# Kernel optimization log

Hardware: AMD Instinct MI355X
Metric: run time of the kernel (lower is better)

Reference implementation:

```python
import jax, jax.numpy as jnp
import numpy as np

N_NODES = 50000
N_EDGES = 800000
IN_FEATS = 128
H_FEATS = 256


def setup_inputs() -> dict:
    key = jax.random.key(0)
    ks = jax.random.split(key, 10)
    in_feat = jax.random.normal(ks[0], (N_NODES, IN_FEATS), dtype=jnp.float32)
    src = jax.random.randint(ks[1], (N_EDGES,), 0, N_NODES, dtype=jnp.int32)
    dst = jax.random.randint(ks[2], (N_EDGES,), 0, N_NODES, dtype=jnp.int32)
    s1 = 1.0 / np.sqrt(IN_FEATS)
    s2 = 1.0 / np.sqrt(H_FEATS)
    return {
        "in_feat": in_feat,
        "src": src,
        "dst": dst,
        "W_self1": jax.random.normal(ks[3], (IN_FEATS, H_FEATS), dtype=jnp.float32) * s1,
        "W_neigh1": jax.random.normal(ks[4], (IN_FEATS, H_FEATS), dtype=jnp.float32) * s1,
        "b1": jnp.zeros((H_FEATS,), dtype=jnp.float32),
        "W_self2": jax.random.normal(ks[5], (H_FEATS, H_FEATS), dtype=jnp.float32) * s2,
        "W_neigh2": jax.random.normal(ks[6], (H_FEATS, H_FEATS), dtype=jnp.float32) * s2,
        "b2": jnp.zeros((H_FEATS,), dtype=jnp.float32),
    }


def _sage_conv(h, src, dst, W_self, W_neigh, b, deg_inv):
    # gather neighbor features along edges, mean-reduce into dst nodes
    msg = h[src]                                              # [E, d]
    agg = jax.ops.segment_sum(msg, dst, num_segments=N_NODES)  # [N, d]
    h_neigh = agg * deg_inv                                   # mean aggregation
    return h @ W_self + h_neigh @ W_neigh + b


def reference(in_feat, src, dst, W_self1, W_neigh1, b1, W_self2, W_neigh2, b2):
    # in-degree for mean (zero-degree nodes -> 0 neighbor contribution)
    deg = jax.ops.segment_sum(jnp.ones((N_EDGES,), dtype=jnp.float32), dst,
                              num_segments=N_NODES)
    deg_inv = (1.0 / jnp.maximum(deg, 1.0))[:, None]          # [N, 1]
    h = _sage_conv(in_feat, src, dst, W_self1, W_neigh1, b1, deg_inv)
    h = jax.nn.relu(h)
    h = _sage_conv(h, src, dst, W_self2, W_neigh2, b2, deg_inv)
    return h
```

## Files before the change

### kernel.cpp

```cpp
#include <hip/hip_runtime.h>
#include <hip/hip_bf16.h>
#include <stdint.h>

#define NN 50000
#define NE 800000
#define IN_F 128
#define H_F 256
#define M_PAD 50048

typedef unsigned int uint32;
typedef unsigned short u16;
typedef __attribute__((ext_vector_type(8))) short short8;
typedef __attribute__((ext_vector_type(4))) float floatx4;

__device__ __forceinline__ float bf16_to_f(uint32 bits16) {
    union { uint32 u; float f; } c; c.u = bits16 << 16; return c.f;
}
__device__ __forceinline__ uint32 f_to_bf16(float f) {
    union { float f; uint32 u; } c; c.f = f;
    uint32 u = c.u;
    u += 0x7FFFu + ((u >> 16) & 1u);
    return u >> 16;
}

__device__ __forceinline__ void gload_lds16(const void* g, void* l) {
    __builtin_amdgcn_global_load_lds((__attribute__((address_space(1))) void*)g,
                                     (__attribute__((address_space(3))) void*)l,
                                     16, 0, 0);
}

#define PREP_A (NN * IN_F / 4)
#define PREP_B (256 * 256)
#define PREP_C (256 * 512)
#define PREP_Z (16 + 32)
#define PREP_TOTAL (PREP_A + PREP_B + PREP_C + PREP_Z + NE)

__global__ void prep_kernel(const float* __restrict__ in_feat, u16* __restrict__ inA,
                            const float* __restrict__ Ws1, const float* __restrict__ Wn1,
                            u16* __restrict__ BT1,
                            const float* __restrict__ Ws2, const float* __restrict__ Wn2,
                            u16* __restrict__ BT2,
                            u16* __restrict__ h,
                            const int* __restrict__ dst, int* __restrict__ counts,
                            int* __restrict__ rank) {
    int id = blockIdx.x * 256 + threadIdx.x;
    if (id < PREP_A) {
        float4 v = *((const float4*)in_feat + id);
        ushort4 o;
        o.x = (u16)f_to_bf16(v.x); o.y = (u16)f_to_bf16(v.y);
        o.z = (u16)f_to_bf16(v.z); o.w = (u16)f_to_bf16(v.w);
        *((ushort4*)inA + id) = o;
        return;
    }
    id -= PREP_A;
    if (id < PREP_B) {
        int n = id >> 8, k = id & 255;
        float v = (k < 128) ? Ws1[(size_t)k * H_F + n] : Wn1[(size_t)(k - 128) * H_F + n];
        BT1[(size_t)n * 256 + k] = (u16)f_to_bf16(v);
        return;
    }
    id -= PREP_B;
    if (id < PREP_C) {
        int n = id >> 9, k = id & 511;
        float v = (k < 256) ? Ws2[(size_t)k * H_F + n] : Wn2[(size_t)(k - 256) * H_F + n];
        BT2[(size_t)n * 512 + k] = (u16)f_to_bf16(v);
        return;
    }
    id -= PREP_C;
    if (id < PREP_Z) {
        uint4 z = {0u, 0u, 0u, 0u};
        if (id < 16) *((uint4*)(inA + (size_t)NN * IN_F) + id) = z;
        else         *((uint4*)(h   + (size_t)NN * H_F)  + (id - 16)) = z;
        return;
    }
    id -= PREP_Z;
    if (id < NE) rank[id] = atomicAdd(&counts[dst[id]], 1);
}


__global__ void scan1_kernel(const int* __restrict__ counts, int* __restrict__ row_start,
                             int* __restrict__ partials, int n) {
    __shared__ int s[256];
    int t = threadIdx.x;
    int i = blockIdx.x * 256 + t;
    int x = (i < n) ? counts[i] : 0;
    s[t] = x;
    __syncthreads();
    for (int off = 1; off < 256; off <<= 1) {
        int y = (t >= off) ? s[t - off] : 0;
        __syncthreads();
        s[t] += y;
        __syncthreads();
    }
    if (i < n) row_start[i] = s[t] - x;
    if (t == 255) partials[blockIdx.x] = s[255];
}

__global__ void scan2_kernel(int* __restrict__ partials, int n) {
    __shared__ int s[256];
    int t = threadIdx.x;
    int x = (t < n) ? partials[t] : 0;
    s[t] = x;
    __syncthreads();
    for (int off = 1; off < 256; off <<= 1) {
        int y = (t >= off) ? s[t - off] : 0;
        __syncthreads();
        s[t] += y;
        __syncthreads();
    }
    if (t < n) partials[t] = s[t] - x;
}

__global__ void scan3_kernel(int* __restrict__ row_start, const int* __restrict__ partials,
                             const int* __restrict__ counts,
                             float* __restrict__ deg_inv, int n) {
    int i = blockIdx.x * 256 + threadIdx.x;
    if (i >= n) return;
    row_start[i] += partials[blockIdx.x];
    int c = counts[i];
    deg_inv[i] = 1.0f / (float)(c > 1 ? c : 1);
}

__global__ void scatter_kernel(const int* __restrict__ src, const int* __restrict__ dst,
                               const int* __restrict__ rank, const int* __restrict__ row_start,
                               int* __restrict__ csr_src) {
    int e = blockIdx.x * 256 + threadIdx.x;
    if (e < NE) {
        int d = dst[e];
        csr_src[row_start[d] + rank[e]] = src[e];
    }
}

template<int DW>
__global__ __launch_bounds__(256)
void agg_kernel(const u16* __restrict__ feats, const int* __restrict__ csr_src,
                const int* __restrict__ row_start, const int* __restrict__ counts,
                const float* __restrict__ deg_inv, u16* __restrict__ outp) {
    constexpr int LPR = DW / 4;
    constexpr int EPW = 64 / LPR;
    constexpr int U   = (DW == 64) ? 8 : 16;
    constexpr int EPI = EPW * U;
    const int w = threadIdx.x >> 6, lane = threadIdx.x & 63;
    const int node = blockIdx.x * 4 + w;
    if (node >= NN) return;
    const int start = row_start[node];
    const int cnt   = counts[node];
    const float dinv = deg_inv[node];
    const int g  = lane / LPR;
    const int wo = (lane % LPR) * 4;
    const uint32* ftw = (const uint32*)feats + wo;

    int clampe = cnt > 0 ? cnt - 1 : 0;
    int myidx = csr_src[start + (lane < clampe ? lane : clampe)];
    if (lane >= cnt) myidx = NN;

    float acc[8] = {};
    const int nb = cnt < 64 ? cnt : 64;
    for (int j = 0; j < nb; j += EPI) {
        uint4 x_[U];
#pragma unroll
        for (int u = 0; u < U; ++u) {
            int idx = __shfl(myidx, j + u * EPW + g);
            x_[u] = *(const uint4*)(ftw + (size_t)idx * DW);
        }
#pragma unroll
        for (int u = 0; u < U; ++u) {
            acc[0] += bf16_to_f(x_[u].x & 0xFFFFu); acc[1] += bf16_to_f(x_[u].x >> 16);
            acc[2] += bf16_to_f(x_[u].y & 0xFFFFu); acc[3] += bf16_to_f(x_[u].y >> 16);
            acc[4] += bf16_to_f(x_[u].z & 0xFFFFu); acc[5] += bf16_to_f(x_[u].z >> 16);
            acc[6] += bf16_to_f(x_[u].w & 0xFFFFu); acc[7] += bf16_to_f(x_[u].w >> 16);
        }
    }
    for (int j = 64; j < cnt; j += EPW) {
        int e = j + g;
        int idx = (e < cnt) ? csr_src[start + e] : NN;
        uint4 x = *(const uint4*)(ftw + (size_t)idx * DW);
        acc[0] += bf16_to_f(x.x & 0xFFFFu); acc[1] += bf16_to_f(x.x >> 16);
        acc[2] += bf16_to_f(x.y & 0xFFFFu); acc[3] += bf16_to_f(x.y >> 16);
        acc[4] += bf16_to_f(x.z & 0xFFFFu); acc[5] += bf16_to_f(x.z >> 16);
        acc[6] += bf16_to_f(x.w & 0xFFFFu); acc[7] += bf16_to_f(x.w >> 16);
    }
#pragma unroll
    for (int k = 0; k < 8; ++k) {
        if (LPR <= 16) acc[k] += __shfl_xor(acc[k], 16);
        acc[k] += __shfl_xor(acc[k], 32);
    }
    if (g == 0) {
        uint4 o;
        o.x = f_to_bf16(acc[0] * dinv) | (f_to_bf16(acc[1] * dinv) << 16);
        o.y = f_to_bf16(acc[2] * dinv) | (f_to_bf16(acc[3] * dinv) << 16);
        o.z = f_to_bf16(acc[4] * dinv) | (f_to_bf16(acc[5] * dinv) << 16);
        o.w = f_to_bf16(acc[6] * dinv) | (f_to_bf16(acc[7] * dinv) << 16);
        *(uint4*)((uint32*)outp + (size_t)node * DW + wo) = o;
    }
}

template<int RELU_BF16>
__global__ __launch_bounds__(256)
void gemm_kernel(const u16* __restrict__ A1, const u16* __restrict__ A2, int K1,
                 const u16* __restrict__ BT, const float* __restrict__ bias,
                 void* __restrict__ outp, int M) {
    __shared__ char lds[32768];
    const int tid = threadIdx.x;
    const int w = tid >> 6, lane = tid & 63;
    const int wr = w >> 1, wc = w & 1;
    const int brow = blockIdx.x * 128;
    const int bcol = blockIdx.y * 128;
    const int Ktot = 2 * K1;
    const int NT = Ktot >> 6;
    const int T1 = K1 >> 6;
    const int l15 = lane & 15, l7 = lane & 7, kg = lane >> 4;
    const int srow = w * 8 + (lane >> 3);
    const int scb = (lane & 7) * 16;
    const size_t sA = (size_t)K1 * 2;
    const size_t sB = (size_t)Ktot * 2;

    floatx4 acc[4][4] = {};

    for (int kt = 0; kt < NT; ++kt) {
        const char* Ab; int ka;
        if (kt < T1) { Ab = (const char*)A1; ka = kt * 64; }
        else         { Ab = (const char*)A2; ka = (kt - T1) * 64; }
#pragma unroll
        for (int i = 0; i < 4; ++i) {
            int row = i * 32 + srow;
            const char* g = Ab + (size_t)(brow + row) * sA + ka * 2 + (scb ^ ((row & 7) << 4));
            gload_lds16(g, &lds[i * 4096 + w * 1024]);
        }
#pragma unroll
        for (int i = 0; i < 4; ++i) {
            int row = i * 32 + srow;
            const char* g = (const char*)BT + (size_t)(bcol + row) * sB + kt * 128 + (scb ^ ((row & 7) << 4));
            gload_lds16(g, &lds[16384 + i * 4096 + w * 1024]);
        }
        __syncthreads();
#pragma unroll
        for (int kk = 0; kk < 2; ++kk) {
            short8 a[4], b[4];
            const int cbyte = (kk * 64 + kg * 16) ^ (l7 << 4);
#pragma unroll
            for (int m = 0; m < 4; ++m)
                a[m] = *(const short8*)&lds[(wr * 64 + m * 16 + l15) * 128 + cbyte];
#pragma unroll
            for (int n = 0; n < 4; ++n)
                b[n] = *(const short8*)&lds[16384 + (wc * 64 + n * 16 + l15) * 128 + cbyte];
#pragma unroll
            for (int m = 0; m < 4; ++m)
#pragma unroll
                for (int n = 0; n < 4; ++n)
                    acc[m][n] = __builtin_amdgcn_mfma_f32_16x16x32_bf16(a[m], b[n], acc[m][n], 0, 0, 0);
        }
        __syncthreads();
    }

    const int orow = brow + wr * 64;
    const int ocol = bcol + wc * 64;
#pragma unroll
    for (int m = 0; m < 4; ++m) {
#pragma unroll
        for (int j = 0; j < 4; ++j) {
            int row = orow + m * 16 + kg * 4 + j;
            if (row < M) {
#pragma unroll
                for (int n = 0; n < 4; ++n) {
                    int col = ocol + n * 16 + l15;
                    float v = acc[m][n][j] + bias[col];
                    if (RELU_BF16) {
                        v = fmaxf(v, 0.0f);
                        ((u16*)outp)[(size_t)row * H_F + col] = (u16)f_to_bf16(v);
                    } else {
                        ((float*)outp)[(size_t)row * H_F + col] = v;
                    }
                }
            }
        }
    }
}


extern "C" void kernel_launch(void* const* d_in, const int* in_sizes, int n_in,
                              void* d_out, int out_size, void* d_ws, size_t ws_size,
                              hipStream_t stream) {
    const float* in_feat  = (const float*)d_in[0];
    const int*   src      = (const int*)d_in[1];
    const int*   dst      = (const int*)d_in[2];
    const float* W_self1  = (const float*)d_in[3];
    const float* W_neigh1 = (const float*)d_in[4];
    const float* b1       = (const float*)d_in[5];
    const float* W_self2  = (const float*)d_in[6];
    const float* W_neigh2 = (const float*)d_in[7];
    const float* b2       = (const float*)d_in[8];
    float* out = (float*)d_out;

    char* p = (char*)d_ws;
    auto alloc = [&](size_t bytes) { char* r = p; p += (bytes + 255) & ~(size_t)255; return r; };
    int*   counts    = (int*)alloc((size_t)NN * 4);
    int*   row_start = (int*)alloc((size_t)NN * 4);
    int*   partials  = (int*)alloc(256 * 4);
    float* deg_inv   = (float*)alloc((size_t)NN * 4);
    int*   rank      = (int*)alloc((size_t)NE * 4);
    int*   csr_src   = (int*)alloc((size_t)NE * 4 + 256);
    u16*   inA       = (u16*)alloc((size_t)M_PAD * IN_F * 2);
    u16*   hn1       = (u16*)alloc((size_t)M_PAD * IN_F * 2);
    u16*   h         = (u16*)alloc((size_t)M_PAD * H_F * 2);
    u16*   hn2       = (u16*)alloc((size_t)M_PAD * H_F * 2);
    u16*   BT1       = (u16*)alloc((size_t)256 * 256 * 2);
    u16*   BT2       = (u16*)alloc((size_t)256 * 512 * 2);

    hipMemsetAsync(counts, 0, (size_t)NN * 4, stream);

    prep_kernel<<<(PREP_TOTAL + 255) / 256, 256, 0, stream>>>(
        in_feat, inA, W_self1, W_neigh1, BT1, W_self2, W_neigh2, BT2, h, dst, counts, rank);

    const int SB = (NN + 255) / 256;
    scan1_kernel<<<SB, 256, 0, stream>>>(counts, row_start, partials, NN);
    scan2_kernel<<<1, 256, 0, stream>>>(partials, SB);
    scan3_kernel<<<SB, 256, 0, stream>>>(row_start, partials, counts, deg_inv, NN);
    scatter_kernel<<<(NE + 255) / 256, 256, 0, stream>>>(src, dst, rank, row_start, csr_src);

    agg_kernel<IN_F / 2><<<(NN + 3) / 4, 256, 0, stream>>>(inA, csr_src, row_start, counts, deg_inv, hn1);
    gemm_kernel<1><<<dim3(M_PAD / 128, 2), 256, 0, stream>>>(inA, hn1, 128, BT1, b1, (void*)h, NN);
    agg_kernel<H_F / 2><<<(NN + 3) / 4, 256, 0, stream>>>(h, csr_src, row_start, counts, deg_inv, hn2);
    gemm_kernel<0><<<dim3(M_PAD / 128, 2), 256, 0, stream>>>(h, hn2, 256, BT2, b2, (void*)out, NN);
}
```

Baseline: 213.0 us.

## Split aggregation feature rows into 64-byte chunks across blocks

The mean-aggregation kernel now gives each wavefront one 64-byte slice of a node's feature row instead of the whole row. The grid is multiplied by the chunk count, so a wavefront handles 16 neighbours in parallel with 4 lanes each and up to 64 in four unrolled loads. The goal is more parallelism and more memory requests in flight for the gather. In exchange, row_start, counts, the CSR indices and deg_inv are re-read once per chunk, cross-lane reductions grow from two shuffle steps to four, and each gather touches only 64 bytes of a neighbour's row.

```diff
diff --git a/kernel.cpp b/kernel.cpp
--- a/kernel.cpp
+++ b/kernel.cpp
@@ -131,47 +131,47 @@
     }
 }
 
-template<int DW>
+template<int DW, int NCHUNK>
 __global__ __launch_bounds__(256)
 void agg_kernel(const u16* __restrict__ feats, const int* __restrict__ csr_src,
                 const int* __restrict__ row_start, const int* __restrict__ counts,
                 const float* __restrict__ deg_inv, u16* __restrict__ outp) {
-    constexpr int LPR = DW / 4;
-    constexpr int EPW = 64 / LPR;
-    constexpr int U   = (DW == 64) ? 8 : 16;
-    constexpr int EPI = EPW * U;
+    constexpr int CHUNKW = DW / NCHUNK;
+    static_assert(CHUNKW == 16, "chunk must be 64B");
     const int w = threadIdx.x >> 6, lane = threadIdx.x & 63;
-    const int node = blockIdx.x * 4 + w;
+    const int c = blockIdx.x % NCHUNK;
+    const int node = (blockIdx.x / NCHUNK) * 4 + w;
     if (node >= NN) return;
     const int start = row_start[node];
     const int cnt   = counts[node];
     const float dinv = deg_inv[node];
-    const int g  = lane / LPR;
-    const int wo = (lane % LPR) * 4;
-    const uint32* ftw = (const uint32*)feats + wo;
+    const int g  = lane >> 2;
+    const int wo = lane & 3;
+    const uint32* ftw = (const uint32*)feats + (size_t)c * CHUNKW + wo * 4;
 
     int clampe = cnt > 0 ? cnt - 1 : 0;
     int myidx = csr_src[start + (lane < clampe ? lane : clampe)];
     if (lane >= cnt) myidx = NN;
 
     float acc[8] = {};
-    const int nb = cnt < 64 ? cnt : 64;
-    for (int j = 0; j < nb; j += EPI) {
-        uint4 x_[U];
-#pragma unroll
-        for (int u = 0; u < U; ++u) {
-            int idx = __shfl(myidx, j + u * EPW + g);
+    uint4 x_[4];
+#pragma unroll
+    for (int u = 0; u < 4; ++u) {
+        if (u * 16 < cnt) {
+            int idx = __shfl(myidx, u * 16 + g);
             x_[u] = *(const uint4*)(ftw + (size_t)idx * DW);
         }
-#pragma unroll
-        for (int u = 0; u < U; ++u) {
+    }
+#pragma unroll
+    for (int u = 0; u < 4; ++u) {
+        if (u * 16 < cnt) {
             acc[0] += bf16_to_f(x_[u].x & 0xFFFFu); acc[1] += bf16_to_f(x_[u].x >> 16);
             acc[2] += bf16_to_f(x_[u].y & 0xFFFFu); acc[3] += bf16_to_f(x_[u].y >> 16);
             acc[4] += bf16_to_f(x_[u].z & 0xFFFFu); acc[5] += bf16_to_f(x_[u].z >> 16);
             acc[6] += bf16_to_f(x_[u].w & 0xFFFFu); acc[7] += bf16_to_f(x_[u].w >> 16);
         }
     }
-    for (int j = 64; j < cnt; j += EPW) {
+    for (int j = 64; j < cnt; j += 16) {
         int e = j + g;
         int idx = (e < cnt) ? csr_src[start + e] : NN;
         uint4 x = *(const uint4*)(ftw + (size_t)idx * DW);
@@ -182,7 +182,9 @@
     }
 #pragma unroll
     for (int k = 0; k < 8; ++k) {
-        if (LPR <= 16) acc[k] += __shfl_xor(acc[k], 16);
+        acc[k] += __shfl_xor(acc[k], 4);
+        acc[k] += __shfl_xor(acc[k], 8);
+        acc[k] += __shfl_xor(acc[k], 16);
         acc[k] += __shfl_xor(acc[k], 32);
     }
     if (g == 0) {
@@ -191,7 +193,7 @@
         o.y = f_to_bf16(acc[2] * dinv) | (f_to_bf16(acc[3] * dinv) << 16);
         o.z = f_to_bf16(acc[4] * dinv) | (f_to_bf16(acc[5] * dinv) << 16);
         o.w = f_to_bf16(acc[6] * dinv) | (f_to_bf16(acc[7] * dinv) << 16);
-        *(uint4*)((uint32*)outp + (size_t)node * DW + wo) = o;
+        *(uint4*)((uint32*)outp + (size_t)node * DW + (size_t)c * CHUNKW + wo * 4) = o;
     }
 }
 
@@ -318,8 +320,9 @@
     scan3_kernel<<<SB, 256, 0, stream>>>(row_start, partials, counts, deg_inv, NN);
     scatter_kernel<<<(NE + 255) / 256, 256, 0, stream>>>(src, dst, rank, row_start, csr_src);
 
-    agg_kernel<IN_F / 2><<<(NN + 3) / 4, 256, 0, stream>>>(inA, csr_src, row_start, counts, deg_inv, hn1);
+    const int NB = (NN + 3) / 4;
+    agg_kernel<IN_F / 2, 4><<<NB * 4, 256, 0, stream>>>(inA, csr_src, row_start, counts, deg_inv, hn1);
     gemm_kernel<1><<<dim3(M_PAD / 128, 2), 256, 0, stream>>>(inA, hn1, 128, BT1, b1, (void*)h, NN);
-    agg_kernel<H_F / 2><<<(NN + 3) / 4, 256, 0, stream>>>(h, csr_src, row_start, counts, deg_inv, hn2);
+    agg_kernel<H_F / 2, 8><<<NB * 8, 256, 0, stream>>>(h, csr_src, row_start, counts, deg_inv, hn2);
     gemm_kernel<0><<<dim3(M_PAD / 128, 2), 256, 0, stream>>>(h, hn2, 256, BT2, b2, (void*)out, NN);
 }
```

Result: slower. 355.0 us (+66.7%).

## Use persistent grid-stride aggregation and full-width 128x256 GEMM tiles

Applied to the files above, without the earlier changes.

The aggregation kernel becomes persistent: 1024 blocks grid-stride over nodes, the unroll is fixed at 16 and gathers are predicated per edge. The GEMM kernel now computes all 256 output columns per block, loading the whole B tile into 48KB of LDS so each A tile is loaded once instead of twice. This cuts launch and block-scheduling overhead and redundant A traffic, at the cost of higher register and LDS use per block, which lowers occupancy, and half as many GEMM blocks.

```diff
diff --git a/kernel.cpp b/kernel.cpp
--- a/kernel.cpp
+++ b/kernel.cpp
@@ -138,60 +138,67 @@
                 const float* __restrict__ deg_inv, u16* __restrict__ outp) {
     constexpr int LPR = DW / 4;
     constexpr int EPW = 64 / LPR;
-    constexpr int U   = (DW == 64) ? 8 : 16;
+    constexpr int U   = 16;
     constexpr int EPI = EPW * U;
     const int w = threadIdx.x >> 6, lane = threadIdx.x & 63;
-    const int node = blockIdx.x * 4 + w;
-    if (node >= NN) return;
-    const int start = row_start[node];
-    const int cnt   = counts[node];
-    const float dinv = deg_inv[node];
+    const int wid = blockIdx.x * 4 + w;
+    const int nw  = gridDim.x * 4;
     const int g  = lane / LPR;
     const int wo = (lane % LPR) * 4;
     const uint32* ftw = (const uint32*)feats + wo;
 
-    int clampe = cnt > 0 ? cnt - 1 : 0;
-    int myidx = csr_src[start + (lane < clampe ? lane : clampe)];
-    if (lane >= cnt) myidx = NN;
-
-    float acc[8] = {};
-    const int nb = cnt < 64 ? cnt : 64;
-    for (int j = 0; j < nb; j += EPI) {
-        uint4 x_[U];
-#pragma unroll
-        for (int u = 0; u < U; ++u) {
-            int idx = __shfl(myidx, j + u * EPW + g);
-            x_[u] = *(const uint4*)(ftw + (size_t)idx * DW);
-        }
-#pragma unroll
-        for (int u = 0; u < U; ++u) {
-            acc[0] += bf16_to_f(x_[u].x & 0xFFFFu); acc[1] += bf16_to_f(x_[u].x >> 16);
-            acc[2] += bf16_to_f(x_[u].y & 0xFFFFu); acc[3] += bf16_to_f(x_[u].y >> 16);
-            acc[4] += bf16_to_f(x_[u].z & 0xFFFFu); acc[5] += bf16_to_f(x_[u].z >> 16);
-            acc[6] += bf16_to_f(x_[u].w & 0xFFFFu); acc[7] += bf16_to_f(x_[u].w >> 16);
-        }
-    }
-    for (int j = 64; j < cnt; j += EPW) {
-        int e = j + g;
-        int idx = (e < cnt) ? csr_src[start + e] : NN;
-        uint4 x = *(const uint4*)(ftw + (size_t)idx * DW);
-        acc[0] += bf16_to_f(x.x & 0xFFFFu); acc[1] += bf16_to_f(x.x >> 16);
-        acc[2] += bf16_to_f(x.y & 0xFFFFu); acc[3] += bf16_to_f(x.y >> 16);
-        acc[4] += bf16_to_f(x.z & 0xFFFFu); acc[5] += bf16_to_f(x.z >> 16);
-        acc[6] += bf16_to_f(x.w & 0xFFFFu); acc[7] += bf16_to_f(x.w >> 16);
-    }
-#pragma unroll
-    for (int k = 0; k < 8; ++k) {
-        if (LPR <= 16) acc[k] += __shfl_xor(acc[k], 16);
-        acc[k] += __shfl_xor(acc[k], 32);
-    }
-    if (g == 0) {
-        uint4 o;
-        o.x = f_to_bf16(acc[0] * dinv) | (f_to_bf16(acc[1] * dinv) << 16);
-        o.y = f_to_bf16(acc[2] * dinv) | (f_to_bf16(acc[3] * dinv) << 16);
-        o.z = f_to_bf16(acc[4] * dinv) | (f_to_bf16(acc[5] * dinv) << 16);
-        o.w = f_to_bf16(acc[6] * dinv) | (f_to_bf16(acc[7] * dinv) << 16);
-        *(uint4*)((uint32*)outp + (size_t)node * DW + wo) = o;
+    for (int node = wid; node < NN; node += nw) {
+        const int start = row_start[node];
+        const int cnt   = counts[node];
+        const float dinv = deg_inv[node];
+
+        int clampe = cnt > 0 ? cnt - 1 : 0;
+        int myidx = csr_src[start + (lane < clampe ? lane : clampe)];
+        if (lane >= cnt) myidx = NN;
+
+        float acc[8] = {};
+        const int nb = cnt < 64 ? cnt : 64;
+        for (int j = 0; j < nb; j += EPI) {
+            uint4 x_[U];
+#pragma unroll
+            for (int u = 0; u < U; ++u) {
+                if (j + u * EPW < cnt) {
+                    int idx = __shfl(myidx, j + u * EPW + g);
+                    x_[u] = *(const uint4*)(ftw + (size_t)idx * DW);
+                }
+            }
+#pragma unroll
+            for (int u = 0; u < U; ++u) {
+                if (j + u * EPW < cnt) {
+                    acc[0] += bf16_to_f(x_[u].x & 0xFFFFu); acc[1] += bf16_to_f(x_[u].x >> 16);
+                    acc[2] += bf16_to_f(x_[u].y & 0xFFFFu); acc[3] += bf16_to_f(x_[u].y >> 16);
+                    acc[4] += bf16_to_f(x_[u].z & 0xFFFFu); acc[5] += bf16_to_f(x_[u].z >> 16);
+                    acc[6] += bf16_to_f(x_[u].w & 0xFFFFu); acc[7] += bf16_to_f(x_[u].w >> 16);
+                }
+            }
+        }
+        for (int j = 64; j < cnt; j += EPW) {
+            int e = j + g;
+            int idx = (e < cnt) ? csr_src[start + e] : NN;
+            uint4 x = *(const uint4*)(ftw + (size_t)idx * DW);
+            acc[0] += bf16_to_f(x.x & 0xFFFFu); acc[1] += bf16_to_f(x.x >> 16);
+            acc[2] += bf16_to_f(x.y & 0xFFFFu); acc[3] += bf16_to_f(x.y >> 16);
+            acc[4] += bf16_to_f(x.z & 0xFFFFu); acc[5] += bf16_to_f(x.z >> 16);
+            acc[6] += bf16_to_f(x.w & 0xFFFFu); acc[7] += bf16_to_f(x.w >> 16);
+        }
+#pragma unroll
+        for (int k = 0; k < 8; ++k) {
+            if (LPR <= 16) acc[k] += __shfl_xor(acc[k], 16);
+            acc[k] += __shfl_xor(acc[k], 32);
+        }
+        if (g == 0) {
+            uint4 o;
+            o.x = f_to_bf16(acc[0] * dinv) | (f_to_bf16(acc[1] * dinv) << 16);
+            o.y = f_to_bf16(acc[2] * dinv) | (f_to_bf16(acc[3] * dinv) << 16);
+            o.z = f_to_bf16(acc[4] * dinv) | (f_to_bf16(acc[5] * dinv) << 16);
+            o.w = f_to_bf16(acc[6] * dinv) | (f_to_bf16(acc[7] * dinv) << 16);
+            *(uint4*)((uint32*)outp + (size_t)node * DW + wo) = o;
+        }
     }
 }
 
@@ -200,12 +207,11 @@
 void gemm_kernel(const u16* __restrict__ A1, const u16* __restrict__ A2, int K1,
                  const u16* __restrict__ BT, const float* __restrict__ bias,
                  void* __restrict__ outp, int M) {
-    __shared__ char lds[32768];
+    __shared__ char lds[49152];
     const int tid = threadIdx.x;
     const int w = tid >> 6, lane = tid & 63;
     const int wr = w >> 1, wc = w & 1;
     const int brow = blockIdx.x * 128;
-    const int bcol = blockIdx.y * 128;
     const int Ktot = 2 * K1;
     const int NT = Ktot >> 6;
     const int T1 = K1 >> 6;
@@ -215,7 +221,7 @@
     const size_t sA = (size_t)K1 * 2;
     const size_t sB = (size_t)Ktot * 2;
 
-    floatx4 acc[4][4] = {};
+    floatx4 acc[2][4][4] = {};
 
     for (int kt = 0; kt < NT; ++kt) {
         const char* Ab; int ka;
@@ -228,48 +234,55 @@
             gload_lds16(g, &lds[i * 4096 + w * 1024]);
         }
 #pragma unroll
-        for (int i = 0; i < 4; ++i) {
+        for (int i = 0; i < 8; ++i) {
             int row = i * 32 + srow;
-            const char* g = (const char*)BT + (size_t)(bcol + row) * sB + kt * 128 + (scb ^ ((row & 7) << 4));
+            const char* g = (const char*)BT + (size_t)row * sB + kt * 128 + (scb ^ ((row & 7) << 4));
             gload_lds16(g, &lds[16384 + i * 4096 + w * 1024]);
         }
         __syncthreads();
 #pragma unroll
         for (int kk = 0; kk < 2; ++kk) {
-            short8 a[4], b[4];
             const int cbyte = (kk * 64 + kg * 16) ^ (l7 << 4);
+            short8 a[4];
 #pragma unroll
             for (int m = 0; m < 4; ++m)
                 a[m] = *(const short8*)&lds[(wr * 64 + m * 16 + l15) * 128 + cbyte];
 #pragma unroll
-            for (int n = 0; n < 4; ++n)
-                b[n] = *(const short8*)&lds[16384 + (wc * 64 + n * 16 + l15) * 128 + cbyte];
-#pragma unroll
-            for (int m = 0; m < 4; ++m)
+            for (int nb = 0; nb < 2; ++nb) {
+                short8 b[4];
 #pragma unroll
                 for (int n = 0; n < 4; ++n)
-                    acc[m][n] = __builtin_amdgcn_mfma_f32_16x16x32_bf16(a[m], b[n], acc[m][n], 0, 0, 0);
+                    b[n] = *(const short8*)&lds[16384 + (nb * 128 + wc * 64 + n * 16 + l15) * 128 + cbyte];
+#pragma unroll
+                for (int m = 0; m < 4; ++m)
+#pragma unroll
+                    for (int n = 0; n < 4; ++n)
+                        acc[nb][m][n] = __builtin_amdgcn_mfma_f32_16x16x32_bf16(a[m], b[n], acc[nb][m][n], 0, 0, 0);
+            }
         }
         __syncthreads();
     }
 
     const int orow = brow + wr * 64;
-    const int ocol = bcol + wc * 64;
-#pragma unroll
-    for (int m = 0; m < 4; ++m) {
-#pragma unroll
-        for (int j = 0; j < 4; ++j) {
-            int row = orow + m * 16 + kg * 4 + j;
-            if (row < M) {
-#pragma unroll
-                for (int n = 0; n < 4; ++n) {
-                    int col = ocol + n * 16 + l15;
-                    float v = acc[m][n][j] + bias[col];
-                    if (RELU_BF16) {
-                        v = fmaxf(v, 0.0f);
-                        ((u16*)outp)[(size_t)row * H_F + col] = (u16)f_to_bf16(v);
-                    } else {
-                        ((float*)outp)[(size_t)row * H_F + col] = v;
+#pragma unroll
+    for (int nb = 0; nb < 2; ++nb) {
+        const int ocol = nb * 128 + wc * 64;
+#pragma unroll
+        for (int m = 0; m < 4; ++m) {
+#pragma unroll
+            for (int j = 0; j < 4; ++j) {
+                int row = orow + m * 16 + kg * 4 + j;
+                if (row < M) {
+#pragma unroll
+                    for (int n = 0; n < 4; ++n) {
+                        int col = ocol + n * 16 + l15;
+                        float v = acc[nb][m][n][j] + bias[col];
+                        if (RELU_BF16) {
+                            v = fmaxf(v, 0.0f);
+                            ((u16*)outp)[(size_t)row * H_F + col] = (u16)f_to_bf16(v);
+                        } else {
+                            ((float*)outp)[(size_t)row * H_F + col] = v;
+                        }
                     }
                 }
             }
@@ -318,8 +331,8 @@
     scan3_kernel<<<SB, 256, 0, stream>>>(row_start, partials, counts, deg_inv, NN);
     scatter_kernel<<<(NE + 255) / 256, 256, 0, stream>>>(src, dst, rank, row_start, csr_src);
 
-    agg_kernel<IN_F / 2><<<(NN + 3) / 4, 256, 0, stream>>>(inA, csr_src, row_start, counts, deg_inv, hn1);
-    gemm_kernel<1><<<dim3(M_PAD / 128, 2), 256, 0, stream>>>(inA, hn1, 128, BT1, b1, (void*)h, NN);
-    agg_kernel<H_F / 2><<<(NN + 3) / 4, 256, 0, stream>>>(h, csr_src, row_start, counts, deg_inv, hn2);
-    gemm_kernel<0><<<dim3(M_PAD / 128, 2), 256, 0, stream>>>(h, hn2, 256, BT2, b2, (void*)out, NN);
-}
+    agg_kernel<IN_F / 2><<<1024, 256, 0, stream>>>(inA, csr_src, row_start, counts, deg_inv, hn1);
+    gemm_kernel<1><<<M_PAD / 128, 256, 0, stream>>>(inA, hn1, 128, BT1, b1, (void*)h, NN);
+    agg_kernel<H_F / 2><<<1024, 256, 0, stream>>>(h, csr_src, row_start, counts, deg_inv, hn2);
+    gemm_kernel<0><<<M_PAD / 128, 256, 0, stream>>>(h, hn2, 256, BT2, b2, (void*)out, NN);
+}
```

Result: slower. 233.1 us (+9.5%).

## Retile GEMM to 64x256 blocks and fold scan2 into scan3

Applied to the files above, without the earlier changes.

The GEMM now gives each block 64 rows and all 256 output columns, so every A row tile is loaded once instead of twice, while the full weight slab is loaded into LDS per K step. Each block holds more B data (LDS grows to 40 KB), which can lower occupancy and raises B traffic per block. Separately, the middle scan kernel is removed: every scan3 block rescans the block partials itself to find its offset, saving one launch at the cost of redundant work in each block.

```diff
diff --git a/kernel.cpp b/kernel.cpp
--- a/kernel.cpp
+++ b/kernel.cpp
@@ -96,10 +96,12 @@
     if (t == 255) partials[blockIdx.x] = s[255];
 }
 
-__global__ void scan2_kernel(int* __restrict__ partials, int n) {
+__global__ void scan3_kernel(int* __restrict__ row_start, const int* __restrict__ partials,
+                             const int* __restrict__ counts,
+                             float* __restrict__ deg_inv, int n, int nparts) {
     __shared__ int s[256];
     int t = threadIdx.x;
-    int x = (t < n) ? partials[t] : 0;
+    int x = (t < nparts) ? partials[t] : 0;
     s[t] = x;
     __syncthreads();
     for (int off = 1; off < 256; off <<= 1) {
@@ -108,15 +110,10 @@
         s[t] += y;
         __syncthreads();
     }
-    if (t < n) partials[t] = s[t] - x;
-}
-
-__global__ void scan3_kernel(int* __restrict__ row_start, const int* __restrict__ partials,
-                             const int* __restrict__ counts,
-                             float* __restrict__ deg_inv, int n) {
-    int i = blockIdx.x * 256 + threadIdx.x;
+    int boff = blockIdx.x ? s[blockIdx.x - 1] : 0;
+    int i = blockIdx.x * 256 + t;
     if (i >= n) return;
-    row_start[i] += partials[blockIdx.x];
+    row_start[i] += boff;
     int c = counts[i];
     deg_inv[i] = 1.0f / (float)(c > 1 ? c : 1);
 }
@@ -200,12 +197,10 @@
 void gemm_kernel(const u16* __restrict__ A1, const u16* __restrict__ A2, int K1,
                  const u16* __restrict__ BT, const float* __restrict__ bias,
                  void* __restrict__ outp, int M) {
-    __shared__ char lds[32768];
+    __shared__ char lds[40960];
     const int tid = threadIdx.x;
     const int w = tid >> 6, lane = tid & 63;
-    const int wr = w >> 1, wc = w & 1;
-    const int brow = blockIdx.x * 128;
-    const int bcol = blockIdx.y * 128;
+    const int brow = blockIdx.x * 64;
     const int Ktot = 2 * K1;
     const int NT = Ktot >> 6;
     const int T1 = K1 >> 6;
@@ -222,16 +217,16 @@
         if (kt < T1) { Ab = (const char*)A1; ka = kt * 64; }
         else         { Ab = (const char*)A2; ka = (kt - T1) * 64; }
 #pragma unroll
-        for (int i = 0; i < 4; ++i) {
+        for (int i = 0; i < 2; ++i) {
             int row = i * 32 + srow;
             const char* g = Ab + (size_t)(brow + row) * sA + ka * 2 + (scb ^ ((row & 7) << 4));
             gload_lds16(g, &lds[i * 4096 + w * 1024]);
         }
 #pragma unroll
-        for (int i = 0; i < 4; ++i) {
+        for (int i = 0; i < 8; ++i) {
             int row = i * 32 + srow;
-            const char* g = (const char*)BT + (size_t)(bcol + row) * sB + kt * 128 + (scb ^ ((row & 7) << 4));
-            gload_lds16(g, &lds[16384 + i * 4096 + w * 1024]);
+            const char* g = (const char*)BT + (size_t)row * sB + kt * 128 + (scb ^ ((row & 7) << 4));
+            gload_lds16(g, &lds[8192 + i * 4096 + w * 1024]);
         }
         __syncthreads();
 #pragma unroll
@@ -240,10 +235,10 @@
             const int cbyte = (kk * 64 + kg * 16) ^ (l7 << 4);
 #pragma unroll
             for (int m = 0; m < 4; ++m)
-                a[m] = *(const short8*)&lds[(wr * 64 + m * 16 + l15) * 128 + cbyte];
+                a[m] = *(const short8*)&lds[(m * 16 + l15) * 128 + cbyte];
 #pragma unroll
             for (int n = 0; n < 4; ++n)
-                b[n] = *(const short8*)&lds[16384 + (wc * 64 + n * 16 + l15) * 128 + cbyte];
+                b[n] = *(const short8*)&lds[8192 + (w * 64 + n * 16 + l15) * 128 + cbyte];
 #pragma unroll
             for (int m = 0; m < 4; ++m)
 #pragma unroll
@@ -253,17 +248,16 @@
         __syncthreads();
     }
 
-    const int orow = brow + wr * 64;
-    const int ocol = bcol + wc * 64;
+    const int ocol0 = w * 64;
 #pragma unroll
     for (int m = 0; m < 4; ++m) {
 #pragma unroll
         for (int j = 0; j < 4; ++j) {
-            int row = orow + m * 16 + kg * 4 + j;
+            int row = brow + m * 16 + kg * 4 + j;
             if (row < M) {
 #pragma unroll
                 for (int n = 0; n < 4; ++n) {
-                    int col = ocol + n * 16 + l15;
+                    int col = ocol0 + n * 16 + l15;
                     float v = acc[m][n][j] + bias[col];
                     if (RELU_BF16) {
                         v = fmaxf(v, 0.0f);
@@ -314,12 +308,11 @@
 
     const int SB = (NN + 255) / 256;
     scan1_kernel<<<SB, 256, 0, stream>>>(counts, row_start, partials, NN);
-    scan2_kernel<<<1, 256, 0, stream>>>(partials, SB);
-    scan3_kernel<<<SB, 256, 0, stream>>>(row_start, partials, counts, deg_inv, NN);
+    scan3_kernel<<<SB, 256, 0, stream>>>(row_start, partials, counts, deg_inv, NN, SB);
     scatter_kernel<<<(NE + 255) / 256, 256, 0, stream>>>(src, dst, rank, row_start, csr_src);
 
     agg_kernel<IN_F / 2><<<(NN + 3) / 4, 256, 0, stream>>>(inA, csr_src, row_start, counts, deg_inv, hn1);
-    gemm_kernel<1><<<dim3(M_PAD / 128, 2), 256, 0, stream>>>(inA, hn1, 128, BT1, b1, (void*)h, NN);
+    gemm_kernel<1><<<M_PAD / 64, 256, 0, stream>>>(inA, hn1, 128, BT1, b1, (void*)h, NN);
     agg_kernel<H_F / 2><<<(NN + 3) / 4, 256, 0, stream>>>(h, csr_src, row_start, counts, deg_inv, hn2);
-    gemm_kernel<0><<<dim3(M_PAD / 128, 2), 256, 0, stream>>>(h, hn2, 256, BT2, b2, (void*)out, NN);
-}
+    gemm_kernel<0><<<M_PAD / 64, 256, 0, stream>>>(h, hn2, 256, BT2, b2, (void*)out, NN);
+}
```

Result: no change. 211.9 us, median of 2 (-0.5%).
